# Kernel tuning notes

Hardware: AMD Instinct MI355X
Metric: run time of the kernel (lower is better)

## Reference

```python
import jax, jax.numpy as jnp
import numpy as np

B, S, H, HEADS = 2, 2048, 1024, 16
KD = H // HEADS          # key_dim = 64
VDIM = 2 * H             # double_v_dim
HD = VDIM // HEADS       # head_size = 128
EPS = 1e-5


def _rotate_every_two(x):
    x1 = x[..., ::2]
    x2 = x[..., 1::2]
    return jnp.stack((-x2, x1), axis=-1).reshape(x.shape)


def _theta_shift(x, sin, cos):
    return x * cos + _rotate_every_two(x) * sin


def setup_inputs() -> dict:
    key = jax.random.key(0)
    ks = jax.random.split(key, 8)
    x = jax.random.normal(ks[0], (B, S, H), dtype=jnp.float32)
    # RoPE-style angles over key_dim, each frequency repeated twice
    half = jnp.arange(KD // 2, dtype=jnp.float32)
    angle = 1.0 / (10000.0 ** (half / (KD // 2)))
    angle = jnp.repeat(angle, 2)                      # [KD]
    pos = jnp.arange(S, dtype=jnp.float32)[:, None]   # [S,1]
    sin = jnp.sin(pos * angle[None, :])               # [S,KD]
    cos = jnp.cos(pos * angle[None, :])
    # per-head exponential decay mask (RetNet)
    decay = 1.0 - 2.0 ** (-5.0 - jnp.arange(HEADS, dtype=jnp.float32))  # [heads]
    i = jnp.arange(S, dtype=jnp.float32)[:, None]
    j = jnp.arange(S, dtype=jnp.float32)[None, :]
    diff = i - j                                       # [S,S]
    logd = jnp.log(decay)[:, None, None]               # [heads,1,1]
    mask = jnp.where(diff[None] >= 0, jnp.exp(logd * diff[None]), 0.0).astype(jnp.float32)
    gain = 0.02
    Wq = gain * jax.random.normal(ks[1], (H, H), dtype=jnp.float32)
    Wk = gain * jax.random.normal(ks[2], (H, H), dtype=jnp.float32)
    Wv = gain * jax.random.normal(ks[3], (VDIM, H), dtype=jnp.float32)
    Wg = gain * jax.random.normal(ks[4], (VDIM, H), dtype=jnp.float32)
    Wo = gain * jax.random.normal(ks[5], (H, VDIM), dtype=jnp.float32)
    return {"x": x, "sin": sin, "cos": cos, "mask": mask,
            "Wq": Wq, "Wk": Wk, "Wv": Wv, "Wg": Wg, "Wo": Wo}


def reference(x, sin, cos, mask, Wq, Wk, Wv, Wg, Wo):
    b, s, h = x.shape
    heads = mask.shape[0]
    kd = h // heads
    vdim = Wv.shape[0]
    hd = vdim // heads
    scaling = kd ** -0.5

    q = jnp.einsum('bsh,oh->bso', x, Wq)
    k = jnp.einsum('bsh,oh->bso', x, Wk) * scaling
    v = jnp.einsum('bsh,oh->bso', x, Wv)
    g = jnp.einsum('bsh,oh->bso', x, Wg)

    q = q.reshape(b, s, heads, kd).transpose(0, 2, 1, 3)  # [b,h,s,kd]
    k = k.reshape(b, s, heads, kd).transpose(0, 2, 1, 3)
    qr = _theta_shift(q, sin, cos)
    kr = _theta_shift(k, sin, cos)

    vr = v.reshape(b, s, heads, hd).transpose(0, 2, 1, 3)  # [b,h,s,hd]

    qk = jnp.einsum('bhsk,bhtk->bhst', qr, kr) * mask      # [b,h,s,s]
    denom = jnp.maximum(jnp.abs(jax.lax.stop_gradient(qk).sum(-1, keepdims=True)), 1.0)
    qk = qk / denom

    out = jnp.einsum('bhst,bhtd->bhsd', qk, vr)            # [b,h,s,hd]
    out = out.transpose(0, 2, 1, 3)                        # [b,s,h,hd]
    # RMSNorm over head_size, no affine, eps=1e-5
    out = out * jax.lax.rsqrt(jnp.mean(out * out, axis=-1, keepdims=True) + EPS)
    out = out.reshape(b, s, heads * hd)                    # [b,s,vdim]
    out = (g * jax.nn.sigmoid(g)) * out                    # swish gate
    return jnp.einsum('bsv,ov->bso', out, Wo)
```

## Files before the change

### kernel.cpp

```cpp
#include <hip/hip_runtime.h>

typedef _Float16 f16;
typedef _Float16 f16x2 __attribute__((ext_vector_type(2)));
typedef _Float16 f16x4 __attribute__((ext_vector_type(4)));
typedef _Float16 f16x8 __attribute__((ext_vector_type(8)));
typedef float f32x4 __attribute__((ext_vector_type(4)));

#define MFMA_16x16x32(a, b, c) __builtin_amdgcn_mfma_f32_16x16x32_f16((a), (b), (c), 0, 0, 0)


__device__ __forceinline__ void async_ld16(const void* g, void* l) {
  __builtin_amdgcn_global_load_lds((const __attribute__((address_space(1))) unsigned int*)g,
                                   (__attribute__((address_space(3))) unsigned int*)l,
                                   16, 0, 0);
}

__global__ void k_cast_all(const float* __restrict__ x, const float* __restrict__ Wq,
                           const float* __restrict__ Wk, const float* __restrict__ Wv,
                           const float* __restrict__ Wg, const float* __restrict__ Wo,
                           f16* __restrict__ xh, f16* __restrict__ W1h, f16* __restrict__ Woh) {
  size_t u = ((size_t)blockIdx.x * 256 + threadIdx.x) * 4;
  const float* src;
  f16* dst;
  float sc = 1.0f;
  if (u < 4194304) {
    src = x + u; dst = xh + u;
  } else if (u < 10485760) {
    size_t idx = u - 4194304;
    int row = (int)(idx >> 10), col = (int)(idx & 1023);
    if (row < 1024)      { src = Wq + (size_t)row * 1024 + col; }
    else if (row < 2048) { src = Wk + (size_t)(row - 1024) * 1024 + col; sc = 0.125f; }
    else if (row < 4096) { src = Wv + (size_t)(row - 2048) * 1024 + col; }
    else                 { src = Wg + (size_t)(row - 4096) * 1024 + col; }
    dst = W1h + idx;
  } else {
    size_t idx = u - 10485760;
    src = Wo + idx; dst = Woh + idx;
  }
  float4 v = *(const float4*)src;
  f16x4 r = { (f16)(v.x * sc), (f16)(v.y * sc), (f16)(v.z * sc), (f16)(v.w * sc) };
  *(f16x4*)dst = r;
}

template <int NT, typename OutT>
__global__ __launch_bounds__(256, 2)
void k_gemm_bt(const f16* __restrict__ A, const f16* __restrict__ Bw,
               OutT* __restrict__ C, int M, int N, int K) {
  __shared__ f16 As[128 * 64];
  __shared__ f16 Bs[NT * 64];
  constexpr int NR = NT / 16;
  const int tid = threadIdx.x;
  const int lane = tid & 63, w = tid >> 6;
  const int quad = lane >> 4, rm = lane & 15;
  const int mt = blockIdx.y, nt = blockIdx.x;
  const f16* Ab = A + (size_t)mt * 128 * K;
  const f16* Bb = Bw + (size_t)nt * NT * K;
  f32x4 acc[2][NR] = {};

  const int sr = lane >> 3;
  const int sc8 = (lane & 7) * 8;

  for (int k0 = 0; k0 < K; k0 += 64) {
    __syncthreads();
#pragma unroll
    for (int p = 0; p < 4; ++p) {
      int br = w * 32 + p * 8;
      async_ld16(Ab + (size_t)(br + sr) * K + k0 + sc8, &As[br * 64]);
    }
#pragma unroll
    for (int p = 0; p < NT / 32; ++p) {
      int br = w * (NT / 4) + p * 8;
      async_ld16(Bb + (size_t)(br + sr) * K + k0 + sc8, &Bs[br * 64]);
    }
    __syncthreads();
#pragma unroll
    for (int kk = 0; kk < 64; kk += 32) {
      const int ko = kk + quad * 8;
      f16x8 a0 = *(const f16x8*)(&As[(w * 32 + rm) * 64 + ko]);
      f16x8 a1 = *(const f16x8*)(&As[(w * 32 + 16 + rm) * 64 + ko]);
#pragma unroll
      for (int n = 0; n < NR; ++n) {
        f16x8 bf = *(const f16x8*)(&Bs[(n * 16 + rm) * 64 + ko]);
        acc[0][n] = MFMA_16x16x32(a0, bf, acc[0][n]);
        acc[1][n] = MFMA_16x16x32(a1, bf, acc[1][n]);
      }
    }
  }
#pragma unroll
  for (int m = 0; m < 2; ++m)
#pragma unroll
    for (int n = 0; n < NR; ++n)
#pragma unroll
      for (int r = 0; r < 4; ++r) {
        int row = mt * 128 + w * 32 + m * 16 + quad * 4 + r;
        int col = nt * NT + n * 16 + rm;
        C[(size_t)row * N + col] = (OutT)acc[m][n][r];
      }
}

__global__ void k_rope(f16* __restrict__ qkvg, const float* __restrict__ sinp,
                       const float* __restrict__ cosp) {
  int u = blockIdx.x * 256 + threadIdx.x;
  int row = u >> 10;
  int col = (u & 1023) * 2;
  int s = row & 2047;
  int d = col & 63;
  f16x2* p = (f16x2*)(qkvg + (size_t)row * 6144 + col);
  f16x2 xv = *p;
  float xe = (float)xv[0], xo = (float)xv[1];
  float se = sinp[s * 64 + d], so = sinp[s * 64 + d + 1];
  float ce = cosp[s * 64 + d], co = cosp[s * 64 + d + 1];
  f16x2 r = { (f16)(xe * ce - xo * se), (f16)(xo * co + xe * so) };
  *p = r;
}

__device__ __forceinline__ int vt_off(int d) { return d * 40 + (d >> 3) * 8; }

__global__ __launch_bounds__(256, 4)
void k_attn(const f16* __restrict__ qkvg, f16* __restrict__ act) {
  constexpr int LDK = 72;
  constexpr int LDP = 40;
  __shared__ f16 Ks[32 * LDK];
  __shared__ f16 Vt[5240];
  __shared__ f16 Ps[4][16 * LDP];
  const int tid = threadIdx.x;
  const int lane = tid & 63, w = tid >> 6;
  const int quad = lane >> 4, rm = lane & 15;
  int bx = blockIdx.x;
  if (blockIdx.z) bx = 31 - bx;
  const int h = blockIdx.y, b = blockIdx.z;
  const int s_blk = bx * 64;
  const size_t ld = 6144;
  const f16* base = qkvg + (size_t)b * 2048 * ld;
  const float logd = logf(1.0f - exp2f(-5.0f - (float)h));

  f16x8 qa[2];
  {
    int row = s_blk + w * 16 + rm;
#pragma unroll
    for (int kh = 0; kh < 2; ++kh)
      qa[kh] = *(const f16x8*)(base + (size_t)row * ld + h * 64 + kh * 32 + quad * 8);
  }
  int voff[8];
#pragma unroll
  for (int n = 0; n < 8; ++n) voff[n] = vt_off(n * 16 + rm) + quad * 8;

  f32x4 od[8];
#pragma unroll
  for (int n = 0; n < 8; ++n) od[n] = (f32x4){0.f, 0.f, 0.f, 0.f};
  float den[4] = {0.f, 0.f, 0.f, 0.f};

  const int tmax = s_blk + 64;
  for (int t0 = 0; t0 < tmax; t0 += 32) {
    __syncthreads();
    {
      int r = tid >> 3, c = (tid & 7) * 8;
      *(uint4*)(&Ks[r * LDK + c]) =
          *(const uint4*)(base + (size_t)(t0 + r) * ld + 1024 + h * 64 + c);
    }
#pragma unroll
    for (int p = 0; p < 2; ++p) {
      int t = p * 16 + (tid >> 4);
      int d0 = (tid & 15) * 8;
      f16x8 v = *(const f16x8*)(base + (size_t)(t0 + t) * ld + 2048 + h * 128 + d0);
#pragma unroll
      for (int j = 0; j < 8; ++j) Vt[vt_off(d0 + j) + t] = v[j];
    }
    __syncthreads();

    f32x4 st[2];
#pragma unroll
    for (int ts = 0; ts < 2; ++ts) st[ts] = (f32x4){0.f, 0.f, 0.f, 0.f};
#pragma unroll
    for (int ts = 0; ts < 2; ++ts) {
      f16x8 bk0 = *(const f16x8*)(&Ks[(ts * 16 + rm) * LDK + quad * 8]);
      f16x8 bk1 = *(const f16x8*)(&Ks[(ts * 16 + rm) * LDK + 32 + quad * 8]);
      st[ts] = MFMA_16x16x32(qa[0], bk0, st[ts]);
      st[ts] = MFMA_16x16x32(qa[1], bk1, st[ts]);
    }
#pragma unroll
    for (int ts = 0; ts < 2; ++ts)
#pragma unroll
      for (int r = 0; r < 4; ++r) {
        int s = s_blk + w * 16 + quad * 4 + r;
        int t = t0 + ts * 16 + rm;
        int diff = s - t;
        float pv = 0.f;
        if (diff >= 0) pv = st[ts][r] * expf(logd * (float)diff);
        den[r] += pv;
        Ps[w][(quad * 4 + r) * LDP + ts * 16 + rm] = (f16)pv;
      }
    __syncthreads();
    f16x8 pa = *(const f16x8*)(&Ps[w][rm * LDP + quad * 8]);
#pragma unroll
    for (int n = 0; n < 8; ++n) {
      f16x8 bv = *(const f16x8*)(&Vt[voff[n]]);
      od[n] = MFMA_16x16x32(pa, bv, od[n]);
    }
  }

  float dn[4], rr[4];
#pragma unroll
  for (int r = 0; r < 4; ++r) {
    float d = den[r];
    d += __shfl_xor(d, 1, 16);
    d += __shfl_xor(d, 2, 16);
    d += __shfl_xor(d, 4, 16);
    d += __shfl_xor(d, 8, 16);
    dn[r] = fmaxf(fabsf(d), 1.0f);
  }
  float ssq[4] = {0.f, 0.f, 0.f, 0.f};
#pragma unroll
  for (int n = 0; n < 8; ++n)
#pragma unroll
    for (int r = 0; r < 4; ++r) {
      float o = od[n][r] / dn[r];
      od[n][r] = o;
      ssq[r] += o * o;
    }
#pragma unroll
  for (int r = 0; r < 4; ++r) {
    float s2 = ssq[r];
    s2 += __shfl_xor(s2, 1, 16);
    s2 += __shfl_xor(s2, 2, 16);
    s2 += __shfl_xor(s2, 4, 16);
    s2 += __shfl_xor(s2, 8, 16);
    rr[r] = rsqrtf(s2 * (1.0f / 128.0f) + 1e-5f);
  }
#pragma unroll
  for (int n = 0; n < 8; ++n)
#pragma unroll
    for (int r = 0; r < 4; ++r) {
      int s = s_blk + w * 16 + quad * 4 + r;
      int dcol = n * 16 + rm;
      float g = (float)base[(size_t)s * ld + 4096 + h * 128 + dcol];
      float o = od[n][r] * rr[r];
      float a = (g / (1.0f + expf(-g))) * o;
      act[((size_t)b * 2048 + s) * 2048 + h * 128 + dcol] = (f16)a;
    }
}

extern "C" void kernel_launch(void* const* d_in, const int* in_sizes, int n_in,
                              void* d_out, int out_size, void* d_ws, size_t ws_size,
                              hipStream_t stream) {
  const float* x    = (const float*)d_in[0];
  const float* sinp = (const float*)d_in[1];
  const float* cosp = (const float*)d_in[2];
  const float* Wq = (const float*)d_in[4];
  const float* Wk = (const float*)d_in[5];
  const float* Wv = (const float*)d_in[6];
  const float* Wg = (const float*)d_in[7];
  const float* Wo = (const float*)d_in[8];
  float* out = (float*)d_out;

  char* ws = (char*)d_ws;
  f16* xh   = (f16*)(ws);
  f16* W1h  = (f16*)(ws + 8388608);
  f16* Woh  = (f16*)(ws + 20971520);
  f16* qkvg = (f16*)(ws + 25165824);
  f16* acth = (f16*)(ws + 75497472);

  k_cast_all<<<12288, 256, 0, stream>>>(x, Wq, Wk, Wv, Wg, Wo, xh, W1h, Woh);

  k_gemm_bt<128, f16><<<dim3(48, 32), 256, 0, stream>>>(xh, W1h, qkvg, 4096, 6144, 1024);

  k_rope<<<16384, 256, 0, stream>>>(qkvg, sinp, cosp);

  k_attn<<<dim3(32, 16, 2), 256, 0, stream>>>(qkvg, acth);

  k_gemm_bt<64, float><<<dim3(16, 32), 256, 0, stream>>>(acth, Woh, out, 4096, 1024, 2048);
}
```

Baseline: 561.8 us.

## Switch retention attention to chunkwise recurrent form with cross-chunk state scan

Replaces the fully parallel causal retention loop, which iterates over all prior key tiles, with a chunkwise formulation. A new kernel computes per-128-token chunk KV states and decayed key sums, and a scan kernel accumulates the decayed states across chunks. The attention kernel then handles only the intra-chunk part and adds the cross-chunk contribution through MFMAs against the scanned state. This turns quadratic work into roughly linear work, at the cost of two extra launches, workspace traffic for the states, and storing the states in fp16. The serial 16-step scan runs on only 32 blocks.

```diff
diff --git a/kernel.cpp b/kernel.cpp
--- a/kernel.cpp
+++ b/kernel.cpp
@@ -114,10 +114,112 @@
   *p = r;
 }
 
+__device__ __forceinline__ int off136(int d) { return d * 136 + ((d >> 3) << 3); }
+
+__global__ __launch_bounds__(256, 2)
+void k_state(const f16* __restrict__ qkvg, float* __restrict__ Sws, float* __restrict__ skws) {
+  __shared__ f16 Kt[8752];
+  __shared__ f16 Vt[17520];
+  __shared__ float skbuf[4][64];
+  const int tid = threadIdx.x;
+  const int lane = tid & 63, w = tid >> 6;
+  const int quad = lane >> 4, rm = lane & 15;
+  const int c = blockIdx.x, h = blockIdx.y, b = blockIdx.z;
+  const int bh = b * 16 + h;
+  const size_t ld = 6144;
+  const f16* base = qkvg + (size_t)b * 2048 * ld + (size_t)c * 128 * ld;
+  const float logd = logf(1.0f - exp2f(-5.0f - (float)h));
+
+#pragma unroll
+  for (int p = 0; p < 4; ++p) {
+    int tau = p * 32 + (tid >> 3);
+    int kd0 = (tid & 7) * 8;
+    f16x8 kv = *(const f16x8*)(base + (size_t)tau * ld + 1024 + h * 64 + kd0);
+    float g = expf(logd * (float)(127 - tau));
+#pragma unroll
+    for (int j = 0; j < 8; ++j) Kt[off136(kd0 + j) + tau] = (f16)((float)kv[j] * g);
+  }
+#pragma unroll
+  for (int p = 0; p < 8; ++p) {
+    int tau = p * 16 + (tid >> 4);
+    int d0 = (tid & 15) * 8;
+    f16x8 vv = *(const f16x8*)(base + (size_t)tau * ld + 2048 + h * 128 + d0);
+#pragma unroll
+    for (int j = 0; j < 8; ++j) Vt[off136(d0 + j) + tau] = vv[j];
+  }
+  __syncthreads();
+
+  f32x4 acc[2][4] = {};
+#pragma unroll
+  for (int kf = 0; kf < 4; ++kf) {
+    int k0 = kf * 32 + quad * 8;
+    f16x8 av[2];
+#pragma unroll
+    for (int mm = 0; mm < 2; ++mm)
+      av[mm] = *(const f16x8*)(&Vt[off136(w * 32 + mm * 16 + rm) + k0]);
+#pragma unroll
+    for (int n = 0; n < 4; ++n) {
+      f16x8 bk = *(const f16x8*)(&Kt[off136(n * 16 + rm) + k0]);
+#pragma unroll
+      for (int mm = 0; mm < 2; ++mm) acc[mm][n] = MFMA_16x16x32(av[mm], bk, acc[mm][n]);
+    }
+  }
+  float* Sout = Sws + ((size_t)c * 32 + bh) * 8192;
+#pragma unroll
+  for (int mm = 0; mm < 2; ++mm)
+#pragma unroll
+    for (int n = 0; n < 4; ++n)
+#pragma unroll
+      for (int r = 0; r < 4; ++r)
+        Sout[(w * 32 + mm * 16 + quad * 4 + r) * 64 + n * 16 + rm] = acc[mm][n][r];
+
+  {
+    int kd = tid & 63;
+    float p = 0.f;
+    for (int tau = w * 32; tau < w * 32 + 32; ++tau) p += (float)Kt[off136(kd) + tau];
+    skbuf[w][kd] = p;
+  }
+  __syncthreads();
+  if (tid < 64) {
+    float s = skbuf[0][tid] + skbuf[1][tid] + skbuf[2][tid] + skbuf[3][tid];
+    skws[((size_t)c * 32 + bh) * 64 + tid] = s;
+  }
+}
+
+__global__ __launch_bounds__(256, 2)
+void k_scan(const float* __restrict__ Sws, const float* __restrict__ skws,
+            f16* __restrict__ Rtws, float* __restrict__ rktws) {
+  const int bh = blockIdx.x;
+  const int h = bh & 15;
+  const int tid = threadIdx.x;
+  const float logd = logf(1.0f - exp2f(-5.0f - (float)h));
+  const float gC = expf(logd * 128.0f);
+  float R[32];
+#pragma unroll
+  for (int i = 0; i < 32; ++i) R[i] = 0.f;
+  float rk = 0.f;
+  for (int c = 0; c < 16; ++c) {
+    size_t bs = ((size_t)c * 32 + bh) * 8192;
+    f16* rt = Rtws + bs;
+    const float* sp = Sws + bs;
+#pragma unroll
+    for (int i = 0; i < 32; ++i) {
+      rt[tid * 32 + i] = (f16)R[i];
+      R[i] = gC * R[i] + sp[tid * 32 + i];
+    }
+    if (tid < 64) {
+      size_t ks = ((size_t)c * 32 + bh) * 64 + tid;
+      rktws[ks] = rk;
+      rk = gC * rk + skws[ks];
+    }
+  }
+}
+
 __device__ __forceinline__ int vt_off(int d) { return d * 40 + (d >> 3) * 8; }
 
 __global__ __launch_bounds__(256, 4)
-void k_attn(const f16* __restrict__ qkvg, f16* __restrict__ act) {
+void k_attn(const f16* __restrict__ qkvg, const f16* __restrict__ Rtws,
+            const float* __restrict__ rktws, f16* __restrict__ act) {
   constexpr int LDK = 72;
   constexpr int LDP = 40;
   __shared__ f16 Ks[32 * LDK];
@@ -129,7 +231,9 @@
   int bx = blockIdx.x;
   if (blockIdx.z) bx = 31 - bx;
   const int h = blockIdx.y, b = blockIdx.z;
+  const int bh = b * 16 + h;
   const int s_blk = bx * 64;
+  const int c = s_blk >> 7;
   const size_t ld = 6144;
   const f16* base = qkvg + (size_t)b * 2048 * ld;
   const float logd = logf(1.0f - exp2f(-5.0f - (float)h));
@@ -151,12 +255,12 @@
   float den[4] = {0.f, 0.f, 0.f, 0.f};
 
   const int tmax = s_blk + 64;
-  for (int t0 = 0; t0 < tmax; t0 += 32) {
+  for (int t0 = c * 128; t0 < tmax; t0 += 32) {
     __syncthreads();
     {
-      int r = tid >> 3, c = (tid & 7) * 8;
-      *(uint4*)(&Ks[r * LDK + c]) =
-          *(const uint4*)(base + (size_t)(t0 + r) * ld + 1024 + h * 64 + c);
+      int r = tid >> 3, cc = (tid & 7) * 8;
+      *(uint4*)(&Ks[r * LDK + cc]) =
+          *(const uint4*)(base + (size_t)(t0 + r) * ld + 1024 + h * 64 + cc);
     }
 #pragma unroll
     for (int p = 0; p < 2; ++p) {
@@ -197,6 +301,35 @@
       f16x8 bv = *(const f16x8*)(&Vt[voff[n]]);
       od[n] = MFMA_16x16x32(pa, bv, od[n]);
     }
+  }
+
+  {
+    const f16* Rt = Rtws + ((size_t)c * 32 + bh) * 8192;
+    float g1 = expf(logd * (float)(s_blk - c * 128 + w * 16 + rm + 1));
+    f16x8 qg[2];
+#pragma unroll
+    for (int kh = 0; kh < 2; ++kh)
+#pragma unroll
+      for (int j = 0; j < 8; ++j) qg[kh][j] = (f16)((float)qa[kh][j] * g1);
+#pragma unroll
+    for (int n = 0; n < 8; ++n) {
+      f16x8 b0 = *(const f16x8*)(Rt + (size_t)(n * 16 + rm) * 64 + quad * 8);
+      f16x8 b1 = *(const f16x8*)(Rt + (size_t)(n * 16 + rm) * 64 + 32 + quad * 8);
+      od[n] = MFMA_16x16x32(qg[0], b0, od[n]);
+      od[n] = MFMA_16x16x32(qg[1], b1, od[n]);
+    }
+    const float* rkp = rktws + ((size_t)c * 32 + bh) * 64;
+    f16x8 bd0, bd1;
+#pragma unroll
+    for (int j = 0; j < 8; ++j) {
+      bd0[j] = (rm == 0) ? (f16)rkp[quad * 8 + j] : (f16)0.f;
+      bd1[j] = (rm == 0) ? (f16)rkp[32 + quad * 8 + j] : (f16)0.f;
+    }
+    f32x4 sd = (f32x4){0.f, 0.f, 0.f, 0.f};
+    sd = MFMA_16x16x32(qg[0], bd0, sd);
+    sd = MFMA_16x16x32(qg[1], bd1, sd);
+#pragma unroll
+    for (int r = 0; r < 4; ++r) den[r] += sd[r];
   }
 
   float dn[4], rr[4];
@@ -254,11 +387,15 @@
   float* out = (float*)d_out;
 
   char* ws = (char*)d_ws;
-  f16* xh   = (f16*)(ws);
-  f16* W1h  = (f16*)(ws + 8388608);
-  f16* Woh  = (f16*)(ws + 20971520);
-  f16* qkvg = (f16*)(ws + 25165824);
-  f16* acth = (f16*)(ws + 75497472);
+  f16* xh     = (f16*)(ws);
+  f16* W1h    = (f16*)(ws + 8388608);
+  f16* Woh    = (f16*)(ws + 20971520);
+  f16* qkvg   = (f16*)(ws + 25165824);
+  f16* acth   = (f16*)(ws + 75497472);
+  float* Sws  = (float*)(ws + 92274688);
+  f16* Rtws   = (f16*)(ws + 109051904);
+  float* skws = (float*)(ws + 117440512);
+  float* rktws= (float*)(ws + 117571584);
 
   k_cast_all<<<12288, 256, 0, stream>>>(x, Wq, Wk, Wv, Wg, Wo, xh, W1h, Woh);
 
@@ -266,7 +403,9 @@
 
   k_rope<<<16384, 256, 0, stream>>>(qkvg, sinp, cosp);
 
-  k_attn<<<dim3(32, 16, 2), 256, 0, stream>>>(qkvg, acth);
+  k_state<<<dim3(16, 16, 2), 256, 0, stream>>>(qkvg, Sws, skws);
+  k_scan<<<32, 256, 0, stream>>>(Sws, skws, Rtws, rktws);
+  k_attn<<<dim3(32, 16, 2), 256, 0, stream>>>(qkvg, Rtws, rktws, acth);
 
   k_gemm_bt<64, float><<<dim3(16, 32), 256, 0, stream>>>(acth, Woh, out, 4096, 1024, 2048);
 }
```

After: 518.8 us. 1.08x faster.
